# Performance work log

Measured on AMD Instinct MI355X. Metric: run time of the kernel, lower is better.

Reference implementation:

```python
import jax, jax.numpy as jnp
import numpy as np

N = 100000      # nodes
D_IN = 512      # in_size
D_OUT = 512     # out_size
E = 200000      # edges per etype
EPS = 1e-5      # LayerNorm eps


def setup_inputs() -> dict:
    key = jax.random.key(0)
    ks = jax.random.split(key, 10)
    scale = 1.0 / np.sqrt(D_IN)
    inp = {
        "x": jax.random.normal(ks[0], (N, D_IN), jnp.float32),
        "W0": jax.random.normal(ks[1], (D_OUT, D_IN), jnp.float32) * scale,
        "W1": jax.random.normal(ks[2], (D_OUT, D_IN), jnp.float32) * scale,
        "W2": jax.random.normal(ks[3], (D_OUT, D_IN), jnp.float32) * scale,
        "gamma": jnp.ones((D_OUT,), jnp.float32),
        "beta": jnp.zeros((D_OUT,), jnp.float32),
        "src0": jax.random.randint(ks[4], (E,), 0, N, jnp.int32),
        "dst0": jax.random.randint(ks[5], (E,), 0, N, jnp.int32),
        "src1": jax.random.randint(ks[6], (E,), 0, N, jnp.int32),
        "dst1": jax.random.randint(ks[7], (E,), 0, N, jnp.int32),
        "src2": jax.random.randint(ks[8], (E,), 0, N, jnp.int32),
        "dst2": jax.random.randint(ks[9], (E,), 0, N, jnp.int32),
    }
    return inp


def _segment_mean(msgs, dst, n):
    # per-dst-node mean; 0 for nodes with no incoming edges (DGL fn.mean semantics)
    s = jax.ops.segment_sum(msgs, dst, num_segments=n)
    c = jax.ops.segment_sum(jnp.ones((msgs.shape[0],), msgs.dtype), dst, num_segments=n)
    return s / jnp.maximum(c, 1.0)[:, None]


def reference(x, W0, W1, W2, gamma, beta, src0, dst0, src1, dst1, src2, dst2):
    # relation-specific linear transforms, averaged over etypes sharing the src ntype
    h = (x @ W0.T + x @ W1.T + x @ W2.T) / 3.0            # [N, D_OUT]
    # per-etype copy_u / mean aggregation
    a0 = _segment_mean(h[src0], dst0, N)
    a1 = _segment_mean(h[src1], dst1, N)
    a2 = _segment_mean(h[src2], dst2, N)
    # cross-etype 'mean' reducer
    h_agg = (a0 + a1 + a2) / 3.0
    # LayerNorm(ReLU(h_agg))
    a = jax.nn.relu(h_agg)
    mu = jnp.mean(a, axis=-1, keepdims=True)
    var = jnp.mean(jnp.square(a - mu), axis=-1, keepdims=True)
    return (a - mu) * jax.lax.rsqrt(var + EPS) * gamma + beta
```

## Files before the change

kernel.cpp:

```cpp
#include <hip/hip_runtime.h>
#include <cstdint>
#include <cstddef>

#define N_NODES 100000
#define DIM 512
#define NE 200000
#define NBLK 391

typedef __attribute__((ext_vector_type(4))) float floatx4;
typedef __attribute__((ext_vector_type(8))) short shortx8;

__device__ __forceinline__ unsigned short f2bf(float f) {
    union { float f; uint32_t u; } v; v.f = f;
    uint32_t r = v.u + 0x7fff + ((v.u >> 16) & 1);
    return (unsigned short)(r >> 16);
}

__device__ __forceinline__ float bf2f(unsigned short h) {
    union { uint32_t u; float f; } v; v.u = ((uint32_t)h) << 16;
    return v.f;
}

__device__ __forceinline__ void load_lds16(const void* g, void* l) {
    __builtin_amdgcn_global_load_lds(
        (const __attribute__((address_space(1))) uint32_t*)g,
        (__attribute__((address_space(3))) uint32_t*)l, 16, 0, 0);
}

__global__ __launch_bounds__(256) void combine_w_kernel(
    const float* __restrict__ W0, const float* __restrict__ W1,
    const float* __restrict__ W2, unsigned short* __restrict__ Wc) {
    int i = blockIdx.x * 256 + threadIdx.x;
    Wc[i] = f2bf((W0[i] + W1[i] + W2[i]) * (1.0f / 3.0f));
}

__global__ __launch_bounds__(256) void count_kernel(
    const int* __restrict__ d0, const int* __restrict__ d1,
    const int* __restrict__ d2, int* __restrict__ cnt) {
    int t = blockIdx.x * 256 + threadIdx.x;
    if (t >= 3 * NE) return;
    int e = t / NE;
    int i = t - e * NE;
    const int* dp = (e == 0) ? d0 : (e == 1) ? d1 : d2;
    atomicAdd(&cnt[e * N_NODES + dp[i]], 1);
}

__global__ __launch_bounds__(256) void scan1_kernel(
    const int* __restrict__ cnt, int* __restrict__ bsum) {
    int t = threadIdx.x;
    int n = blockIdx.x * 256 + t;
    int rl = 0;
    if (n < N_NODES) rl = cnt[n] + cnt[N_NODES + n] + cnt[2 * N_NODES + n];
    int v = rl;
    #pragma unroll
    for (int off = 32; off > 0; off >>= 1) v += __shfl_xor(v, off);
    __shared__ int ws_[4];
    if ((t & 63) == 0) ws_[t >> 6] = v;
    __syncthreads();
    if (t == 0) bsum[blockIdx.x] = ws_[0] + ws_[1] + ws_[2] + ws_[3];
}

__global__ __launch_bounds__(512) void scan2_kernel(
    const int* __restrict__ bsum, int* __restrict__ boff) {
    __shared__ int sh[512];
    int t = threadIdx.x;
    int v = (t < NBLK) ? bsum[t] : 0;
    sh[t] = v;
    __syncthreads();
    #pragma unroll
    for (int off = 1; off < 512; off <<= 1) {
        int add = (t >= off) ? sh[t - off] : 0;
        __syncthreads();
        sh[t] += add;
        __syncthreads();
    }
    if (t < NBLK) boff[t] = sh[t] - v;
}

__global__ __launch_bounds__(256) void scan3_kernel(
    const int* __restrict__ cnt, const int* __restrict__ boff,
    int* __restrict__ row_start, int* __restrict__ cursor) {
    __shared__ int sh[256];
    int t = threadIdx.x;
    int n = blockIdx.x * 256 + t;
    int rl = 0;
    if (n < N_NODES) rl = cnt[n] + cnt[N_NODES + n] + cnt[2 * N_NODES + n];
    sh[t] = rl;
    __syncthreads();
    #pragma unroll
    for (int off = 1; off < 256; off <<= 1) {
        int add = (t >= off) ? sh[t - off] : 0;
        __syncthreads();
        sh[t] += add;
        __syncthreads();
    }
    if (n < N_NODES) {
        int excl = sh[t] - rl + boff[blockIdx.x];
        row_start[n] = excl;
        cursor[n] = excl;
    }
}

__global__ __launch_bounds__(256) void bin_kernel(
    const int* __restrict__ s0, const int* __restrict__ d0,
    const int* __restrict__ s1, const int* __restrict__ d1,
    const int* __restrict__ s2, const int* __restrict__ d2,
    int* __restrict__ cursor, int* __restrict__ src_tag) {
    int t = blockIdx.x * 256 + threadIdx.x;
    if (t >= 3 * NE) return;
    int e = t / NE;
    int i = t - e * NE;
    const int* sp; const int* dp;
    if (e == 0)      { sp = s0; dp = d0; }
    else if (e == 1) { sp = s1; dp = d1; }
    else             { sp = s2; dp = d2; }
    int d = dp[i];
    int pos = atomicAdd(&cursor[d], 1);
    src_tag[pos] = sp[i] | (e << 30);
}

__global__ __launch_bounds__(256) void gemm_kernel(
    const float* __restrict__ X, const unsigned short* __restrict__ B,
    unsigned short* __restrict__ H, int M) {
    __shared__ alignas(16) unsigned short As[128 * 32];
    __shared__ alignas(16) unsigned short Bs[128 * 32];
    const int tid = threadIdx.x;
    const int lane = tid & 63;
    const int w = tid >> 6;
    const int wr = w >> 1, wc = w & 1;
    const int q = lane >> 4, r = lane & 15;

    int lid = ((int)blockIdx.x & 7) * 391 + ((int)blockIdx.x >> 3);
    int mt = lid >> 2, nt = lid & 3;
    int m0 = mt * 128, n0 = nt * 128;

    int arow0 = tid >> 2, ac8 = tid & 3;
    int gm0 = m0 + arow0;       if (gm0 >= M) gm0 = M - 1;
    int gm1 = m0 + arow0 + 64;  if (gm1 >= M) gm1 = M - 1;
    const float* ap0 = X + (size_t)gm0 * DIM + ac8 * 8;
    const float* ap1 = X + (size_t)gm1 * DIM + ac8 * 8;

    float4 a00, a01, a10, a11;
    #define ALOAD(k0_) do { \
        a00 = *(const float4*)(ap0 + (k0_));     a01 = *(const float4*)(ap0 + (k0_) + 4); \
        a10 = *(const float4*)(ap1 + (k0_));     a11 = *(const float4*)(ap1 + (k0_) + 4); \
    } while (0)

    floatx4 acc[4][4] = {};
    ALOAD(0);

    for (int k0 = 0; k0 < DIM; k0 += 32) {
        #pragma unroll
        for (int i = 0; i < 2; ++i) {
            int cb = i * 256 + tid;
            int row = cb >> 2, c = cb & 3;
            load_lds16(&B[(size_t)(n0 + row) * DIM + k0 + c * 8], &Bs[cb * 8]);
        }
        {
            shortx8 p0, p1;
            p0[0] = f2bf(a00.x); p0[1] = f2bf(a00.y); p0[2] = f2bf(a00.z); p0[3] = f2bf(a00.w);
            p0[4] = f2bf(a01.x); p0[5] = f2bf(a01.y); p0[6] = f2bf(a01.z); p0[7] = f2bf(a01.w);
            p1[0] = f2bf(a10.x); p1[1] = f2bf(a10.y); p1[2] = f2bf(a10.z); p1[3] = f2bf(a10.w);
            p1[4] = f2bf(a11.x); p1[5] = f2bf(a11.y); p1[6] = f2bf(a11.z); p1[7] = f2bf(a11.w);
            *(shortx8*)&As[tid * 8] = p0;
            *(shortx8*)&As[(tid + 256) * 8] = p1;
        }
        __syncthreads();
        if (k0 + 32 < DIM) ALOAD(k0 + 32);

        shortx8 af[4], bfr[4];
        #pragma unroll
        for (int mi = 0; mi < 4; ++mi)
            af[mi] = *(const shortx8*)&As[(wr * 64 + mi * 16 + r) * 32 + q * 8];
        #pragma unroll
        for (int nj = 0; nj < 4; ++nj)
            bfr[nj] = *(const shortx8*)&Bs[(wc * 64 + nj * 16 + r) * 32 + q * 8];
        #pragma unroll
        for (int mi = 0; mi < 4; ++mi)
            #pragma unroll
            for (int nj = 0; nj < 4; ++nj)
                acc[mi][nj] = __builtin_amdgcn_mfma_f32_16x16x32_bf16(
                    af[mi], bfr[nj], acc[mi][nj], 0, 0, 0);
        __syncthreads();
    }
    #undef ALOAD

    #pragma unroll
    for (int mi = 0; mi < 4; ++mi) {
        #pragma unroll
        for (int rg = 0; rg < 4; ++rg) {
            int gm = m0 + wr * 64 + mi * 16 + q * 4 + rg;
            if (gm < M) {
                #pragma unroll
                for (int nj = 0; nj < 4; ++nj)
                    H[(size_t)gm * DIM + n0 + wc * 64 + nj * 16 + r] =
                        f2bf(acc[mi][nj][rg]);
            }
        }
    }
}

__global__ __launch_bounds__(256) void gather_ln_kernel(
    const unsigned short* __restrict__ h, const int* __restrict__ row_start,
    const int* __restrict__ cnt, const int* __restrict__ src_tag,
    const float* __restrict__ gamma, const float* __restrict__ beta,
    float* __restrict__ out) {
    const int lane = threadIdx.x & 63;
    const int n = blockIdx.x * 4 + (threadIdx.x >> 6);
    if (n >= N_NODES) return;
    const int c0 = cnt[n], c1 = cnt[N_NODES + n], c2 = cnt[2 * N_NODES + n];
    const int len = c0 + c1 + c2;
    const float w0 = 1.0f / (3.0f * (float)max(c0, 1));
    const float w1 = 1.0f / (3.0f * (float)max(c1, 1));
    const float w2 = 1.0f / (3.0f * (float)max(c2, 1));
    const int beg = row_start[n];
    const size_t lx = (size_t)lane * 8;
    float acc[8] = {};
    for (int base = 0; base < len; base += 64) {
        int rem = len - base;
        int m = rem < 64 ? rem : 64;
        int tag = (lane < m) ? src_tag[beg + base + lane] : 0;
        int j = 0;
        for (; j + 4 <= m; j += 4) {
            int u0 = __shfl(tag, j),     u1 = __shfl(tag, j + 1);
            int u2 = __shfl(tag, j + 2), u3 = __shfl(tag, j + 3);
            int e0 = ((unsigned)u0) >> 30, e1 = ((unsigned)u1) >> 30;
            int e2 = ((unsigned)u2) >> 30, e3 = ((unsigned)u3) >> 30;
            float g0 = (e0 == 0) ? w0 : ((e0 == 1) ? w1 : w2);
            float g1 = (e1 == 0) ? w0 : ((e1 == 1) ? w1 : w2);
            float g2 = (e2 == 0) ? w0 : ((e2 == 1) ? w1 : w2);
            float g3 = (e3 == 0) ? w0 : ((e3 == 1) ? w1 : w2);
            shortx8 v0 = *(const shortx8*)(h + (size_t)(u0 & 0x3FFFFFFF) * DIM + lx);
            shortx8 v1 = *(const shortx8*)(h + (size_t)(u1 & 0x3FFFFFFF) * DIM + lx);
            shortx8 v2 = *(const shortx8*)(h + (size_t)(u2 & 0x3FFFFFFF) * DIM + lx);
            shortx8 v3 = *(const shortx8*)(h + (size_t)(u3 & 0x3FFFFFFF) * DIM + lx);
            #pragma unroll
            for (int k = 0; k < 8; ++k) {
                acc[k] += bf2f((unsigned short)v0[k]) * g0;
                acc[k] += bf2f((unsigned short)v1[k]) * g1;
                acc[k] += bf2f((unsigned short)v2[k]) * g2;
                acc[k] += bf2f((unsigned short)v3[k]) * g3;
            }
        }
        for (; j < m; ++j) {
            int u = __shfl(tag, j);
            int e = ((unsigned)u) >> 30;
            float wg = (e == 0) ? w0 : ((e == 1) ? w1 : w2);
            shortx8 v = *(const shortx8*)(h + (size_t)(u & 0x3FFFFFFF) * DIM + lx);
            #pragma unroll
            for (int k = 0; k < 8; ++k)
                acc[k] += bf2f((unsigned short)v[k]) * wg;
        }
    }
    float s1_ = 0.0f, s2_ = 0.0f;
    #pragma unroll
    for (int k = 0; k < 8; ++k) {
        float v = fmaxf(acc[k], 0.0f);
        acc[k] = v; s1_ += v; s2_ += v * v;
    }
    #pragma unroll
    for (int off = 1; off < 64; off <<= 1) {
        s1_ += __shfl_xor(s1_, off);
        s2_ += __shfl_xor(s2_, off);
    }
    float mu = s1_ * (1.0f / DIM);
    float var = s2_ * (1.0f / DIM) - mu * mu;
    float rstd = rsqrtf(var + 1e-5f);
    float4 g0 = *(const float4*)(gamma + lane * 8);
    float4 g1 = *(const float4*)(gamma + lane * 8 + 4);
    float4 b0 = *(const float4*)(beta + lane * 8);
    float4 b1 = *(const float4*)(beta + lane * 8 + 4);
    float4 o0, o1;
    o0.x = (acc[0] - mu) * rstd * g0.x + b0.x;
    o0.y = (acc[1] - mu) * rstd * g0.y + b0.y;
    o0.z = (acc[2] - mu) * rstd * g0.z + b0.z;
    o0.w = (acc[3] - mu) * rstd * g0.w + b0.w;
    o1.x = (acc[4] - mu) * rstd * g1.x + b1.x;
    o1.y = (acc[5] - mu) * rstd * g1.y + b1.y;
    o1.z = (acc[6] - mu) * rstd * g1.z + b1.z;
    o1.w = (acc[7] - mu) * rstd * g1.w + b1.w;
    float4* op = (float4*)(out + (size_t)n * DIM + lane * 8);
    op[0] = o0;
    op[1] = o1;
}

extern "C" void kernel_launch(void* const* d_in, const int* in_sizes, int n_in,
                              void* d_out, int out_size, void* d_ws, size_t ws_size,
                              hipStream_t stream) {
    const float* x     = (const float*)d_in[0];
    const float* W0    = (const float*)d_in[1];
    const float* W1    = (const float*)d_in[2];
    const float* W2    = (const float*)d_in[3];
    const float* gamma = (const float*)d_in[4];
    const float* beta  = (const float*)d_in[5];
    const int* s0  = (const int*)d_in[6];
    const int* dd0 = (const int*)d_in[7];
    const int* s1  = (const int*)d_in[8];
    const int* dd1 = (const int*)d_in[9];
    const int* s2  = (const int*)d_in[10];
    const int* dd2 = (const int*)d_in[11];
    float* out = (float*)d_out;

    char* ws = (char*)d_ws;
    size_t off = 0;
    int* cnt = (int*)(ws + off);             off += 3u * N_NODES * 4u;
    int* row_start = (int*)(ws + off);       off += (size_t)N_NODES * 4u;
    int* cursor = (int*)(ws + off);          off += (size_t)N_NODES * 4u;
    int* bsum = (int*)(ws + off);            off += 2048;
    int* boff = (int*)(ws + off);            off += 2048;
    int* src_tag = (int*)(ws + off);         off += (size_t)3 * NE * 4u;
    unsigned short* Wc = (unsigned short*)(ws + off); off += (size_t)DIM * DIM * 2u;
    off = (off + 255) & ~255ull;
    unsigned short* h = (unsigned short*)(ws + off);

    hipMemsetAsync(cnt, 0, (size_t)3 * N_NODES * sizeof(int), stream);

    combine_w_kernel<<<(DIM * DIM) / 256, 256, 0, stream>>>(W0, W1, W2, Wc);
    count_kernel<<<(3 * NE + 255) / 256, 256, 0, stream>>>(dd0, dd1, dd2, cnt);
    scan1_kernel<<<NBLK, 256, 0, stream>>>(cnt, bsum);
    scan2_kernel<<<1, 512, 0, stream>>>(bsum, boff);
    scan3_kernel<<<NBLK, 256, 0, stream>>>(cnt, boff, row_start, cursor);
    bin_kernel<<<(3 * NE + 255) / 256, 256, 0, stream>>>(
        s0, dd0, s1, dd1, s2, dd2, cursor, src_tag);

    gemm_kernel<<<3128, 256, 0, stream>>>(x, Wc, h, N_NODES);

    gather_ln_kernel<<<(N_NODES + 3) / 4, 256, 0, stream>>>(
        h, row_start, cnt, src_tag, gamma, beta, out);
}
```

Baseline: 575.7 us.

## Double GEMM K-tile to 64, use chunk-major LDS layout and packed bf16 conversion

The GEMM main loop now stages K=64 per iteration instead of 32, which halves the number of barrier pairs and global-load rounds. The LDS tiles move from row-major to a chunk-major [kchunk][row] layout, so each lane's 16-byte fragment reads hit consecutive rows and bank conflicts should drop. The fp32-to-bf16 conversion switches from manual rounding to paired hardware conversion intrinsics. In exchange it uses twice the LDS and more A-prefetch registers, which may reduce occupancy.

```diff
diff --git a/kernel.cpp b/kernel.cpp
--- a/kernel.cpp
+++ b/kernel.cpp
@@ -1,4 +1,5 @@
 #include <hip/hip_runtime.h>
+#include <hip/hip_bf16.h>
 #include <cstdint>
 #include <cstddef>
 
@@ -19,6 +20,15 @@
 __device__ __forceinline__ float bf2f(unsigned short h) {
     union { uint32_t u; float f; } v; v.u = ((uint32_t)h) << 16;
     return v.f;
+}
+
+__device__ __forceinline__ shortx8 cvt8(const float4 a, const float4 b) {
+    union { __hip_bfloat162 h2[4]; shortx8 s8; } u;
+    u.h2[0] = __float22bfloat162_rn(make_float2(a.x, a.y));
+    u.h2[1] = __float22bfloat162_rn(make_float2(a.z, a.w));
+    u.h2[2] = __float22bfloat162_rn(make_float2(b.x, b.y));
+    u.h2[3] = __float22bfloat162_rn(make_float2(b.z, b.w));
+    return u.s8;
 }
 
 __device__ __forceinline__ void load_lds16(const void* g, void* l) {
@@ -122,8 +132,8 @@
 __global__ __launch_bounds__(256) void gemm_kernel(
     const float* __restrict__ X, const unsigned short* __restrict__ B,
     unsigned short* __restrict__ H, int M) {
-    __shared__ alignas(16) unsigned short As[128 * 32];
-    __shared__ alignas(16) unsigned short Bs[128 * 32];
+    __shared__ alignas(16) unsigned short As[128 * 64];
+    __shared__ alignas(16) unsigned short Bs[128 * 64];
     const int tid = threadIdx.x;
     const int lane = tid & 63;
     const int w = tid >> 6;
@@ -134,56 +144,57 @@
     int mt = lid >> 2, nt = lid & 3;
     int m0 = mt * 128, n0 = nt * 128;
 
-    int arow0 = tid >> 2, ac8 = tid & 3;
-    int gm0 = m0 + arow0;       if (gm0 >= M) gm0 = M - 1;
-    int gm1 = m0 + arow0 + 64;  if (gm1 >= M) gm1 = M - 1;
-    const float* ap0 = X + (size_t)gm0 * DIM + ac8 * 8;
-    const float* ap1 = X + (size_t)gm1 * DIM + ac8 * 8;
-
-    float4 a00, a01, a10, a11;
-    #define ALOAD(k0_) do { \
-        a00 = *(const float4*)(ap0 + (k0_));     a01 = *(const float4*)(ap0 + (k0_) + 4); \
-        a10 = *(const float4*)(ap1 + (k0_));     a11 = *(const float4*)(ap1 + (k0_) + 4); \
-    } while (0)
+    const float* aptr[4];
+    #pragma unroll
+    for (int i = 0; i < 4; ++i) {
+        int ca = i * 256 + tid;
+        int row = ca & 127, c = ca >> 7;
+        int gm = m0 + row; if (gm >= M) gm = M - 1;
+        aptr[i] = X + (size_t)gm * DIM + c * 8;
+    }
+    float4 areg[4][2];
+    auto aload = [&](int k0_) {
+        #pragma unroll
+        for (int i = 0; i < 4; ++i) {
+            areg[i][0] = *(const float4*)(aptr[i] + k0_);
+            areg[i][1] = *(const float4*)(aptr[i] + k0_ + 4);
+        }
+    };
 
     floatx4 acc[4][4] = {};
-    ALOAD(0);
-
-    for (int k0 = 0; k0 < DIM; k0 += 32) {
-        #pragma unroll
-        for (int i = 0; i < 2; ++i) {
+    aload(0);
+
+    for (int k0 = 0; k0 < DIM; k0 += 64) {
+        #pragma unroll
+        for (int i = 0; i < 4; ++i) {
             int cb = i * 256 + tid;
-            int row = cb >> 2, c = cb & 3;
+            int row = cb & 127, c = cb >> 7;
             load_lds16(&B[(size_t)(n0 + row) * DIM + k0 + c * 8], &Bs[cb * 8]);
         }
-        {
-            shortx8 p0, p1;
-            p0[0] = f2bf(a00.x); p0[1] = f2bf(a00.y); p0[2] = f2bf(a00.z); p0[3] = f2bf(a00.w);
-            p0[4] = f2bf(a01.x); p0[5] = f2bf(a01.y); p0[6] = f2bf(a01.z); p0[7] = f2bf(a01.w);
-            p1[0] = f2bf(a10.x); p1[1] = f2bf(a10.y); p1[2] = f2bf(a10.z); p1[3] = f2bf(a10.w);
-            p1[4] = f2bf(a11.x); p1[5] = f2bf(a11.y); p1[6] = f2bf(a11.z); p1[7] = f2bf(a11.w);
-            *(shortx8*)&As[tid * 8] = p0;
-            *(shortx8*)&As[(tid + 256) * 8] = p1;
-        }
-        __syncthreads();
-        if (k0 + 32 < DIM) ALOAD(k0 + 32);
-
-        shortx8 af[4], bfr[4];
-        #pragma unroll
-        for (int mi = 0; mi < 4; ++mi)
-            af[mi] = *(const shortx8*)&As[(wr * 64 + mi * 16 + r) * 32 + q * 8];
-        #pragma unroll
-        for (int nj = 0; nj < 4; ++nj)
-            bfr[nj] = *(const shortx8*)&Bs[(wc * 64 + nj * 16 + r) * 32 + q * 8];
-        #pragma unroll
-        for (int mi = 0; mi < 4; ++mi)
+        #pragma unroll
+        for (int i = 0; i < 4; ++i)
+            *(shortx8*)&As[(i * 256 + tid) * 8] = cvt8(areg[i][0], areg[i][1]);
+        __syncthreads();
+        if (k0 + 64 < DIM) aload(k0 + 64);
+
+        #pragma unroll
+        for (int kk = 0; kk < 2; ++kk) {
+            shortx8 af[4], bfr[4];
+            #pragma unroll
+            for (int mi = 0; mi < 4; ++mi)
+                af[mi] = *(const shortx8*)&As[((kk * 4 + q) * 128 + wr * 64 + mi * 16 + r) * 8];
             #pragma unroll
             for (int nj = 0; nj < 4; ++nj)
-                acc[mi][nj] = __builtin_amdgcn_mfma_f32_16x16x32_bf16(
-                    af[mi], bfr[nj], acc[mi][nj], 0, 0, 0);
-        __syncthreads();
-    }
-    #undef ALOAD
+                bfr[nj] = *(const shortx8*)&Bs[((kk * 4 + q) * 128 + wc * 64 + nj * 16 + r) * 8];
+            #pragma unroll
+            for (int mi = 0; mi < 4; ++mi)
+                #pragma unroll
+                for (int nj = 0; nj < 4; ++nj)
+                    acc[mi][nj] = __builtin_amdgcn_mfma_f32_16x16x32_bf16(
+                        af[mi], bfr[nj], acc[mi][nj], 0, 0, 0);
+        }
+        __syncthreads();
+    }
 
     #pragma unroll
     for (int mi = 0; mi < 4; ++mi) {
```

After: 632.4 us. 1.1x slower.
